# Kernel optimization log

Hardware: AMD Instinct MI355X
Metric: run time of the kernel (lower is better)

## Reference

```python
import jax, jax.numpy as jnp
import numpy as np
from jax import lax

K_DIM, E_DIM, H_DIM, BETA = 256, 64, 256, 0.25
DN = ('NCHW', 'OIHW', 'NCHW')


def conv(x, w, b=None, stride=1, pad=0):
    y = lax.conv_general_dilated(x, w, (stride, stride), [(pad, pad), (pad, pad)], dimension_numbers=DN)
    if b is not None:
        y = y + b[None, :, None, None]
    return y


def deconv(x, w, b):
    # torch ConvTranspose2d(k=4, stride=2, pad=1): weight [in, out, kH, kW]
    rhs = jnp.flip(w, (2, 3)).swapaxes(0, 1)  # -> [out, in, kH, kW]
    y = lax.conv_general_dilated(x, rhs, (1, 1), [(2, 2), (2, 2)], lhs_dilation=(2, 2), dimension_numbers=DN)
    return y + b[None, :, None, None]


def res_block(x, w3, w1):
    out = jax.nn.relu(x)
    out = conv(out, w3, stride=1, pad=1)
    out = jax.nn.relu(out)
    out = conv(out, w1, stride=1, pad=0)
    return out + x


def vq_embed(z, codebook):
    # z: [B, C, Hs, Ws]; faithful to original: flatten to (-1, e_dim) even though C != e_dim
    zp = jnp.transpose(z, (0, 2, 3, 1))  # [B,Hs,Ws,C]
    zf = zp.reshape(-1, E_DIM)  # [N, e_dim]
    # ||z||^2 + ||e||^2 - 2 z e^T
    dist = (jnp.sum(zf * zf, axis=1, keepdims=True)
            + jnp.sum(codebook * codebook, axis=1)
            - 2.0 * zf @ codebook.T)  # [N, K]
    idx = jnp.argmin(dist, axis=1)  # [N]
    vq = jnp.take(codebook, idx, axis=0).reshape(zp.shape)  # gather == one-hot matmul
    loss = (jnp.mean((lax.stop_gradient(vq) - zp) ** 2)
            + BETA * jnp.mean((vq - lax.stop_gradient(zp)) ** 2))
    vq_st = zp + lax.stop_gradient(vq - zp)  # straight-through
    return loss, jnp.transpose(vq_st, (0, 3, 1, 2))


def setup_inputs() -> dict:
    key = jax.random.key(0)
    ks = jax.random.split(key, 20)
    f32 = jnp.float32
    s = 0.05
    inp = {
        'x': jax.random.normal(ks[0], (32, 3, 128, 128), f32),
        'enc_w1': jax.random.normal(ks[1], (H_DIM, 3, 4, 4), f32) * s,
        'enc_b1': jnp.zeros((H_DIM,), f32),
        'enc_w2': jax.random.normal(ks[2], (H_DIM, H_DIM, 4, 4), f32) * s,
        'enc_b2': jnp.zeros((H_DIM,), f32),
        'er1_w3': jax.random.normal(ks[3], (H_DIM, H_DIM, 3, 3), f32) * s,
        'er1_w1': jax.random.normal(ks[4], (H_DIM, H_DIM, 1, 1), f32) * s,
        'er2_w3': jax.random.normal(ks[5], (H_DIM, H_DIM, 3, 3), f32) * s,
        'er2_w1': jax.random.normal(ks[6], (H_DIM, H_DIM, 1, 1), f32) * s,
        'codebook': jax.random.uniform(ks[7], (K_DIM, E_DIM), f32, -1.0 / K_DIM, 1.0 / K_DIM),
        'dr1_w3': jax.random.normal(ks[8], (H_DIM, H_DIM, 3, 3), f32) * s,
        'dr1_w1': jax.random.normal(ks[9], (H_DIM, H_DIM, 1, 1), f32) * s,
        'dr2_w3': jax.random.normal(ks[10], (H_DIM, H_DIM, 3, 3), f32) * s,
        'dr2_w1': jax.random.normal(ks[11], (H_DIM, H_DIM, 1, 1), f32) * s,
        'dt1_w': jax.random.normal(ks[12], (H_DIM, H_DIM, 4, 4), f32) * s,  # [in,out,k,k]
        'dt1_b': jnp.zeros((H_DIM,), f32),
        'dt2_w': jax.random.normal(ks[13], (H_DIM, 3, 4, 4), f32) * s,
        'dt2_b': jnp.zeros((3,), f32),
    }
    return inp


def reference(x, enc_w1, enc_b1, enc_w2, enc_b2, er1_w3, er1_w1, er2_w3, er2_w1,
              codebook, dr1_w3, dr1_w1, dr2_w3, dr2_w1, dt1_w, dt1_b, dt2_w, dt2_b):
    # encoder
    z = conv(x, enc_w1, enc_b1, stride=2, pad=1)
    z = conv(z, enc_w2, enc_b2, stride=2, pad=1)
    z = res_block(z, er1_w3, er1_w1)
    z = res_block(z, er2_w3, er2_w1)
    # VQ
    emb_loss, vq_z = vq_embed(z, codebook)
    # decoder
    d = res_block(vq_z, dr1_w3, dr1_w1)
    d = res_block(d, dr2_w3, dr2_w1)
    d = deconv(d, dt1_w, dt1_b)
    d = deconv(d, dt2_w, dt2_b)
    recon = jnp.tanh(d)
    return recon, emb_loss
```

## Files before the change

### kernel.cpp

```cpp
#include <hip/hip_runtime.h>
#include <math.h>


typedef unsigned short ushort;
typedef short bf16x8 __attribute__((ext_vector_type(8)));
typedef float f32x4 __attribute__((ext_vector_type(4)));

__device__ __forceinline__ ushort f2bf(float f) {
    unsigned u = __builtin_bit_cast(unsigned, f);
    unsigned r = (u + 0x7fffu + ((u >> 16) & 1u)) >> 16;
    return (ushort)r;
}
__device__ __forceinline__ float bfl(unsigned u) { return __builtin_bit_cast(float, u << 16); }
__device__ __forceinline__ float bfh(unsigned u) { return __builtin_bit_cast(float, u & 0xffff0000u); }

__device__ __forceinline__ unsigned relu_u(unsigned u) {
    unsigned m = (u >> 15) & 0x00010001u;
    return u & ~((m << 16) - m);
}
__device__ __forceinline__ uint4 relu4(uint4 v) {
    v.x = relu_u(v.x); v.y = relu_u(v.y); v.z = relu_u(v.z); v.w = relu_u(v.w);
    return v;
}

__global__ void k_pack_c3x4(const float* __restrict__ w0, const float* __restrict__ w1,
                            const float* __restrict__ w2, const float* __restrict__ w3,
                            ushort* __restrict__ o0, ushort* __restrict__ o1,
                            ushort* __restrict__ o2, ushort* __restrict__ o3) {
    int layer = blockIdx.x / 2304;
    int i = (blockIdx.x - layer * 2304) * 256 + threadIdx.x;
    const float* w = layer == 0 ? w0 : layer == 1 ? w1 : layer == 2 ? w2 : w3;
    ushort* o = layer == 0 ? o0 : layer == 1 ? o1 : layer == 2 ? o2 : o3;
    int kk = i & 31, co = (i >> 5) & 255, cb = (i >> 13) & 7, t = i >> 16;
    int ci = cb * 32 + kk, kh = t / 3, kw = t % 3;
    o[i] = f2bf(w[((co * 256 + ci) * 3 + kh) * 3 + kw]);
}

__global__ void k_pack_c1x1x4(const float* __restrict__ w0, const float* __restrict__ w1,
                              const float* __restrict__ w2, const float* __restrict__ w3,
                              ushort* __restrict__ o0, ushort* __restrict__ o1,
                              ushort* __restrict__ o2, ushort* __restrict__ o3) {
    int layer = blockIdx.x >> 8;
    int i = (blockIdx.x & 255) * 256 + threadIdx.x;
    const float* w = layer == 0 ? w0 : layer == 1 ? w1 : layer == 2 ? w2 : w3;
    ushort* o = layer == 0 ? o0 : layer == 1 ? o1 : layer == 2 ? o2 : o3;
    int kk = i & 31, co = (i >> 5) & 255, cb = (i >> 13) & 7;
    o[i] = f2bf(w[co * 256 + cb * 32 + kk]);
}

__global__ void k_pack_vq(const float* __restrict__ cb, ushort* __restrict__ apk,
                          float* __restrict__ en) {
    if (blockIdx.x < 64) {
        int i = blockIdx.x * 256 + threadIdx.x;
        int j = i & 7, lane = (i >> 3) & 63, s = (i >> 9) & 1, t = i >> 10;
        int code = t * 16 + (lane & 15);
        int dim = s * 32 + (lane >> 4) * 8 + j;
        apk[i] = f2bf(cb[code * 64 + dim]);
    } else {
        int code = threadIdx.x;
        float s = 0.f;
        for (int d = 0; d < 64; ++d) { float v = cb[code * 64 + d]; s += v * v; }
        en[code] = s;
    }
}

__global__ __launch_bounds__(256) void k_wcomp_enc(const float* __restrict__ w1,
                                                   const float* __restrict__ b1f,
                                                   const float* __restrict__ w2,
                                                   const float* __restrict__ b2f,
                                                   ushort* __restrict__ wenc,
                                                   float* __restrict__ benc,
                                                   float* __restrict__ wct,
                                                   float* __restrict__ wcb,
                                                   float* __restrict__ wcl,
                                                   float* __restrict__ wcr,
                                                   float* __restrict__ wcc) {
    __shared__ float sw1[12288];
    __shared__ float sw2[4096];
    __shared__ float part[2400];
    int co = blockIdx.x, tid = threadIdx.x;
    for (int i = tid; i < 12288; i += 256) sw1[i] = w1[i];
    for (int i = tid; i < 4096; i += 256) sw2[i] = w2[co * 4096 + i];
    __syncthreads();

    {
        float s = 0.f;
#pragma unroll
        for (int t = 0; t < 16; ++t) s += sw2[tid * 16 + t];
        float pb = b1f[tid] * s;
#pragma unroll
        for (int m = 1; m < 64; m <<= 1) pb += __shfl_xor(pb, m);
        if ((tid & 63) == 0) part[tid >> 6] = pb;
    }
    __syncthreads();
    if (tid == 0) benc[co] = b2f[co] + part[0] + part[1] + part[2] + part[3];

    if (tid < 240) {
        int y = tid / 24, rem = tid % 24, ci = rem / 8, ms = rem % 8;
        int na = 0, aa[2], h1[2];
#pragma unroll
        for (int a = 0; a < 4; ++a) {
            int k1 = y - 2 * a;
            if ((unsigned)k1 < 4u) { aa[na] = a; h1[na] = k1; ++na; }
        }
        float acc10[10];
#pragma unroll
        for (int xx = 0; xx < 10; ++xx) acc10[xx] = 0.f;
        for (int m = ms * 32; m < ms * 32 + 32; ++m) {
            for (int pa = 0; pa < na; ++pa) {
                float4 a2 = *(const float4*)&sw2[m * 16 + aa[pa] * 4];
                float4 a1 = *(const float4*)&sw1[m * 48 + ci * 16 + h1[pa] * 4];
                acc10[0] += a2.x * a1.x; acc10[1] += a2.x * a1.y; acc10[2] += a2.x * a1.z; acc10[3] += a2.x * a1.w;
                acc10[2] += a2.y * a1.x; acc10[3] += a2.y * a1.y; acc10[4] += a2.y * a1.z; acc10[5] += a2.y * a1.w;
                acc10[4] += a2.z * a1.x; acc10[5] += a2.z * a1.y; acc10[6] += a2.z * a1.z; acc10[7] += a2.z * a1.w;
                acc10[6] += a2.w * a1.x; acc10[7] += a2.w * a1.y; acc10[8] += a2.w * a1.z; acc10[9] += a2.w * a1.w;
            }
        }
#pragma unroll
        for (int xx = 0; xx < 10; ++xx) part[tid * 10 + xx] = acc10[xx];
    }
    __syncthreads();
    for (int w = tid; w < 320; w += 256) {
        if (w < 300) {
            int y = w / 30, r = w % 30, ci = r / 10, xx = r % 10;
            float s = 0.f;
#pragma unroll
            for (int ms = 0; ms < 8; ++ms) s += part[((y * 24 + ci * 8) + ms) * 10 + xx];
            wenc[(y * 256 + co) * 32 + xx * 3 + ci] = f2bf(s);
        } else {
            int j = w - 300;
            int y = j >> 1;
            wenc[(y * 256 + co) * 32 + 30 + (j & 1)] = 0;
        }
    }

    if (tid < 30 || (tid >= 32 && tid < 62)) {
        bool top = tid < 30;
        int t = top ? tid : tid - 32;
        int xx = t / 3, ci = t % 3;
        int k2hf = top ? 0 : 3, k1hf = top ? 3 : 0;
        float s = 0.f;
        for (int m = 0; m < 256; ++m)
            for (int k2w = 0; k2w < 4; ++k2w) {
                int k1w = xx - 2 * k2w;
                if ((unsigned)k1w < 4u)
                    s += sw2[m * 16 + k2hf * 4 + k2w] * sw1[m * 48 + ci * 16 + k1hf * 4 + k1w];
            }
        (top ? wct : wcb)[t * 256 + co] = s;
    } else if ((tid >= 64 && tid < 94) || (tid >= 96 && tid < 126)) {
        bool left = tid < 94;
        int t = left ? tid - 64 : tid - 96;
        int y = t / 3, ci = t % 3;
        int k2wf = left ? 0 : 3, k1wf = left ? 3 : 0;
        float s = 0.f;
        for (int m = 0; m < 256; ++m)
            for (int k2h = 0; k2h < 4; ++k2h) {
                int k1h = y - 2 * k2h;
                if ((unsigned)k1h < 4u)
                    s += sw2[m * 16 + k2h * 4 + k2wf] * sw1[m * 48 + ci * 16 + k1h * 4 + k1wf];
            }
        (left ? wcl : wcr)[t * 256 + co] = s;
    } else if (tid >= 128 && tid < 140) {
        int c = (tid - 128) / 3, ci = (tid - 128) % 3;
        int k2h = (c >> 1) ? 3 : 0, k2w = (c & 1) ? 3 : 0;
        int k1h = 3 - k2h, k1w = 3 - k2w;
        float s = 0.f;
        for (int m = 0; m < 256; ++m)
            s += sw2[m * 16 + k2h * 4 + k2w] * sw1[m * 48 + ci * 16 + k1h * 4 + k1w];
        wcc[(c * 3 + ci) * 256 + co] = s;
    }
}

__global__ __launch_bounds__(256) void k_wcomp_dec(const float* __restrict__ dt1,
                                                   const float* __restrict__ dt1b,
                                                   const float* __restrict__ dt2,
                                                   const float* __restrict__ dt2b,
                                                   ushort* __restrict__ wdec,
                                                   float* __restrict__ bdec) {
    __shared__ float s1[4096];
    __shared__ float s2[12288];
    __shared__ float part[2400];
    int ci = blockIdx.x, tid = threadIdx.x;
    for (int i = tid; i < 4096; i += 256) s1[i] = dt1[ci * 4096 + i];
    for (int i = tid; i < 12288; i += 256) s2[i] = dt2[i];
    __syncthreads();

    if (ci == 0 && tid < 48) {
        int o = tid >> 4, p = tid & 15, py = p >> 2, px = p & 3;
        int c0 = (py + 1) & 1, d0 = (px + 1) & 1;
        float s = dt2b[o];
        for (int m = 0; m < 256; ++m) {
            float t2 = s2[m * 48 + o * 16 + c0 * 4 + d0] + s2[m * 48 + o * 16 + c0 * 4 + d0 + 2]
                     + s2[m * 48 + o * 16 + (c0 + 2) * 4 + d0] + s2[m * 48 + o * 16 + (c0 + 2) * 4 + d0 + 2];
            s += dt1b[m] * t2;
        }
        bdec[tid] = s;
    }

    if (tid < 240) {
        int y = tid / 24, rem = tid % 24, o = rem / 8, ms = rem % 8;
        int na = 0, aa[2], cc[2];
#pragma unroll
        for (int a = 0; a < 4; ++a) {
            int c = y - 2 * a;
            if ((unsigned)c < 4u) { aa[na] = a; cc[na] = c; ++na; }
        }
        float acc10[10];
#pragma unroll
        for (int xx = 0; xx < 10; ++xx) acc10[xx] = 0.f;
        for (int m = ms * 32; m < ms * 32 + 32; ++m) {
            for (int pa = 0; pa < na; ++pa) {
                float4 d1 = *(const float4*)&s1[m * 16 + aa[pa] * 4];
                float4 d2 = *(const float4*)&s2[m * 48 + o * 16 + cc[pa] * 4];
                acc10[0] += d1.x * d2.x; acc10[1] += d1.x * d2.y; acc10[2] += d1.x * d2.z; acc10[3] += d1.x * d2.w;
                acc10[2] += d1.y * d2.x; acc10[3] += d1.y * d2.y; acc10[4] += d1.y * d2.z; acc10[5] += d1.y * d2.w;
                acc10[4] += d1.z * d2.x; acc10[5] += d1.z * d2.y; acc10[6] += d1.z * d2.z; acc10[7] += d1.z * d2.w;
                acc10[6] += d1.w * d2.x; acc10[7] += d1.w * d2.y; acc10[8] += d1.w * d2.z; acc10[9] += d1.w * d2.w;
            }
        }
#pragma unroll
        for (int xx = 0; xx < 10; ++xx) part[tid * 10 + xx] = acc10[xx];
    }
    __syncthreads();
    for (int w = tid; w < 300; w += 256) {
        int y = w / 30, r = w % 30, o = r / 10, xx = r % 10;
        float s = 0.f;
#pragma unroll
        for (int ms = 0; ms < 8; ++ms) s += part[((y * 24 + o * 8) + ms) * 10 + xx];
        int du = (y < 3) ? 1 : (y < 7) ? 0 : -1;
        int py = y - 3 + 4 * du;
        int dv = (xx < 3) ? 1 : (xx < 7) ? 0 : -1;
        int px = xx - 3 + 4 * dv;
        int t = (du + 1) * 3 + (dv + 1);
        int cb2 = ci >> 5, kk = ci & 31;
        wdec[((((t * 3 + o) * 8 + cb2) * 16 + py * 4 + px) * 32) + kk] = f2bf(s);
    }
}

__global__ void k_xpack(const float* __restrict__ x, ushort* __restrict__ xpk) {
    int i = blockIdx.x * 256 + threadIdx.x;
    int k = i & 31, ow = (i >> 5) & 31, r = (i >> 10) & 127, n = i >> 17;
    float v = 0.f;
    if (k < 30) {
        int ci = k % 3, kw = k / 3;
        int col = 4 * ow - 3 + kw;
        if ((unsigned)col < 128u) v = x[((n * 3 + ci) * 128 + r) * 128 + col];
    }
    xpk[i] = f2bf(v);
}

__global__ __launch_bounds__(128) void k_enc_comp(const ushort* __restrict__ xpk,
                                                  const ushort* __restrict__ wenc,
                                                  const float* __restrict__ benc,
                                                  ushort* __restrict__ obf) {
    int tid = threadIdx.x, lane = tid & 63, wv = tid >> 6;
    int q = lane >> 4, l15 = lane & 15;
    int b = blockIdx.x;
    int mblk = b & 7, coslab = (b >> 3) & 3, n = b >> 5;
    int R0 = mblk * 4 + wv * 2;
    int aoff = (coslab * 64 + l15) * 32 + q * 8;

    f32x4 acc[4][4];
#pragma unroll
    for (int at = 0; at < 4; ++at)
#pragma unroll
        for (int bt = 0; bt < 4; ++bt) acc[at][bt] = 0.f;

    for (int t = 0; t < 10; ++t) {
        bf16x8 af[4];
#pragma unroll
        for (int at = 0; at < 4; ++at)
            af[at] = *(const bf16x8*)(wenc + t * 8192 + aoff + at * 512);
#pragma unroll
        for (int bt2 = 0; bt2 < 2; ++bt2) {
            int irow = 4 * (R0 + bt2) + t - 3;
            if ((unsigned)irow >= 128u) continue;
            bf16x8 bf[2];
#pragma unroll
            for (int hb = 0; hb < 2; ++hb) {
                int ow = hb * 16 + l15;
                bf[hb] = *(const bf16x8*)(xpk + (((long)n * 128 + irow) * 32 + ow) * 32 + q * 8);
            }
#pragma unroll
            for (int at = 0; at < 4; ++at)
#pragma unroll
                for (int hb = 0; hb < 2; ++hb)
                    acc[at][bt2 * 2 + hb] = __builtin_amdgcn_mfma_f32_16x16x32_bf16(
                        af[at], bf[hb], acc[at][bt2 * 2 + hb], 0, 0, 0);
        }
    }

    int co_base = coslab * 64;
#pragma unroll
    for (int at = 0; at < 4; ++at) {
        int co_t = co_base + at * 16 + q * 4;
        float4 b4 = *(const float4*)(benc + co_t);
        float bv[4] = {b4.x, b4.y, b4.z, b4.w};
#pragma unroll
        for (int bt = 0; bt < 4; ++bt) {
            int m = R0 * 32 + bt * 16 + l15;
            long oaddr = ((long)n * 1024 + m) * 256 + co_t;
            float v[4];
#pragma unroll
            for (int r = 0; r < 4; ++r) v[r] = acc[at][bt][r] + bv[r];
            uint2 pk;
            pk.x = (unsigned)f2bf(v[0]) | ((unsigned)f2bf(v[1]) << 16);
            pk.y = (unsigned)f2bf(v[2]) | ((unsigned)f2bf(v[3]) << 16);
            *(uint2*)(obf + oaddr) = pk;
        }
    }
}

__global__ __launch_bounds__(256) void k_fix_border(const float* __restrict__ x,
                                                    const ushort* __restrict__ xpk,
                                                    const float* __restrict__ wct,
                                                    const float* __restrict__ wcb,
                                                    const float* __restrict__ wcl,
                                                    const float* __restrict__ wcr,
                                                    const float* __restrict__ wcc,
                                                    ushort* __restrict__ X0) {
    int b = blockIdx.x;
    int n = b >> 7, job = b & 127;
    if (job >= 124) return;
    int co = threadIdx.x;

    auto dot_tb = [&](const float* __restrict__ w, int row, int qq) -> float {
        const ushort* xr = xpk + (((long)n * 128 + row) * 32 + qq) * 32;
        float s = 0.f;
        for (int k = 0; k < 30; ++k) s += w[k * 256 + co] * bfl((unsigned)xr[k]);
        return s;
    };
    auto dot_lr = [&](const float* __restrict__ w, int p, int colofs) -> float {
        float s = 0.f;
        for (int y = 0; y < 10; ++y) {
            int row = 4 * p - 3 + y;
            if ((unsigned)row >= 128u) continue;
            for (int ci = 0; ci < 3; ++ci)
                s += w[(y * 3 + ci) * 256 + co] * x[((long)(n * 3 + ci) * 128 + row) * 128 + colofs];
        }
        return s;
    };
    auto corner = [&](int c, int row, int colofs) -> float {
        float s = 0.f;
        for (int ci = 0; ci < 3; ++ci)
            s += wcc[(c * 3 + ci) * 256 + co] * x[((long)(n * 3 + ci) * 128 + row) * 128 + colofs];
        return s;
    };

    int m;
    float corr;
    if (job < 32) {
        int qq = job;
        m = qq;
        corr = dot_tb(wct, 0, qq);
        if (qq == 0)  corr += dot_lr(wcl, 0, 0)   - corner(0, 0, 0);
        if (qq == 31) corr += dot_lr(wcr, 0, 127) - corner(1, 0, 127);
    } else if (job < 64) {
        int qq = job - 32;
        m = 992 + qq;
        corr = dot_tb(wcb, 127, qq);
        if (qq == 0)  corr += dot_lr(wcl, 31, 0)   - corner(2, 127, 0);
        if (qq == 31) corr += dot_lr(wcr, 31, 127) - corner(3, 127, 127);
    } else if (job < 94) {
        int p = job - 63;
        m = 32 * p;
        corr = dot_lr(wcl, p, 0);
    } else {
        int p = job - 93;
        m = 32 * p + 31;
        corr = dot_lr(wcr, p, 127);
    }

    ushort* ptr = X0 + ((long)n * 1024 + m) * 256 + co;
    float v = bfl((unsigned)(*ptr));
    *ptr = f2bf(v - corr);
}

__global__ __launch_bounds__(256, 2) void k_resblock(const ushort* __restrict__ xin,
                                                     const ushort* __restrict__ w3pk,
                                                     const ushort* __restrict__ w1pk,
                                                     ushort* __restrict__ obf) {
    constexpr int BUFU = 4 * 4 * 34 * 8;
    __shared__ __align__(16) ushort sX[2 * BUFU];
    __shared__ __align__(16) ushort sEx[64 * 256];

    int tid = threadIdx.x, lane = tid & 63, wv = tid >> 6;
    int q = lane >> 4, l15 = lane & 15;
    int b = blockIdx.x;
    int rp = b & 15, n = b >> 4;
    int R0 = rp * 2;

    if (tid < 64) {
        int bufi = tid >> 5, rq = (tid >> 1) & 15, cc = (tid & 1) ? 33 : 0;
        uint4 z; z.x = z.y = z.z = z.w = 0;
        *(uint4*)&sX[bufi * BUFU + (rq * 34 + cc) * 8] = z;
    }

    int brr[4], bcol[4];
#pragma unroll
    for (int bt = 0; bt < 4; ++bt) {
        int p = bt * 16 + l15;
        brr[bt] = p >> 5; bcol[bt] = (p & 31) + 1;
    }

    int scol = lane >> 1, j0 = (lane & 1) * 2;
    int aoff = (wv * 64 + l15) * 32 + q * 8;

    f32x4 acc[4][4];
#pragma unroll
    for (int at = 0; at < 4; ++at)
#pragma unroll
        for (int bt = 0; bt < 4; ++bt) acc[at][bt] = 0.f;

    int hh = R0 - 1 + wv;
    bool hvalid = (unsigned)hh < 32u;
    uint4 sreg[2];
    auto stage_load = [&](int cb2) {
        long off = (((long)n * 32 + hh) * 32 + scol) * 256 + cb2 * 32 + j0 * 8;
#pragma unroll
        for (int k = 0; k < 2; ++k) {
            uint4 v;
            if (hvalid) v = relu4(*(const uint4*)(xin + off + k * 8));
            else { v.x = 0; v.y = 0; v.z = 0; v.w = 0; }
            sreg[k] = v;
        }
    };
    auto write_stage = [&](int pbuf) {
        ushort* bufp = sX + pbuf * BUFU;
#pragma unroll
        for (int k = 0; k < 2; ++k)
            *(uint4*)&bufp[((wv * 4 + j0 + k) * 34 + scol + 1) * 8] = sreg[k];
    };

    stage_load(0);
    write_stage(0);
    __syncthreads();

    for (int cb = 0; cb < 8; ++cb) {
        ushort* bufp = sX + (cb & 1) * BUFU;
        if (cb + 1 < 8) stage_load(cb + 1);
        const ushort* wb = w3pk + (long)cb * 8192 + aoff;

        bf16x8 afc[4];
#pragma unroll
        for (int at = 0; at < 4; ++at) afc[at] = *(const bf16x8*)(wb + at * 512);
#pragma unroll
        for (int t = 0; t < 9; ++t) {
            bf16x8 afn[4];
            if (t < 8) {
#pragma unroll
                for (int at = 0; at < 4; ++at)
                    afn[at] = *(const bf16x8*)(wb + (long)(t + 1) * 65536 + at * 512);
            }
            int taprow = t / 3, dx = t % 3 - 1;
            bf16x8 bfr[4];
#pragma unroll
            for (int bt = 0; bt < 4; ++bt)
                bfr[bt] = *(const bf16x8*)&bufp[(((brr[bt] + taprow) * 4 + q) * 34 + bcol[bt] + dx) * 8];
#pragma unroll
            for (int at = 0; at < 4; ++at)
#pragma unroll
                for (int bt = 0; bt < 4; ++bt)
                    acc[at][bt] = __builtin_amdgcn_mfma_f32_16x16x32_bf16(afc[at], bfr[bt],
                                                                          acc[at][bt], 0, 0, 0);
            if (t < 8) {
#pragma unroll
                for (int at = 0; at < 4; ++at) afc[at] = afn[at];
            }
        }

        if (cb + 1 < 8) {
            write_stage((cb + 1) & 1);
            __syncthreads();
        }
    }

#pragma unroll
    for (int at = 0; at < 4; ++at) {
        int co_t = wv * 64 + at * 16 + q * 4;
#pragma unroll
        for (int bt = 0; bt < 4; ++bt) {
            int px = bt * 16 + l15;
            uint2 pk;
            pk.x = (unsigned)f2bf(fmaxf(acc[at][bt][0], 0.f))
                 | ((unsigned)f2bf(fmaxf(acc[at][bt][1], 0.f)) << 16);
            pk.y = (unsigned)f2bf(fmaxf(acc[at][bt][2], 0.f))
                 | ((unsigned)f2bf(fmaxf(acc[at][bt][3], 0.f)) << 16);
            *(uint2*)&sEx[px * 256 + (co_t ^ ((px & 7) << 3))] = pk;
        }
    }
    __syncthreads();

    f32x4 acc2[4][4];
#pragma unroll
    for (int at = 0; at < 4; ++at)
#pragma unroll
        for (int bt = 0; bt < 4; ++bt) acc2[at][bt] = 0.f;

    for (int cb = 0; cb < 8; ++cb) {
        const ushort* wb1 = w1pk + (long)cb * 8192 + aoff;
        bf16x8 af1[4];
#pragma unroll
        for (int at = 0; at < 4; ++at) af1[at] = *(const bf16x8*)(wb1 + at * 512);
        bf16x8 bf1[4];
#pragma unroll
        for (int bt = 0; bt < 4; ++bt) {
            int px = bt * 16 + l15;
            bf1[bt] = *(const bf16x8*)&sEx[px * 256 + ((cb * 32 + q * 8) ^ ((px & 7) << 3))];
        }
#pragma unroll
        for (int at = 0; at < 4; ++at)
#pragma unroll
            for (int bt = 0; bt < 4; ++bt)
                acc2[at][bt] = __builtin_amdgcn_mfma_f32_16x16x32_bf16(af1[at], bf1[bt],
                                                                      acc2[at][bt], 0, 0, 0);
    }

#pragma unroll
    for (int at = 0; at < 4; ++at) {
        int co_t = wv * 64 + at * 16 + q * 4;
#pragma unroll
        for (int bt = 0; bt < 4; ++bt) {
            int m = R0 * 32 + bt * 16 + l15;
            long oaddr = ((long)n * 1024 + m) * 256 + co_t;
            uint2 rr = *(const uint2*)(xin + oaddr);
            float v[4];
            v[0] = acc2[at][bt][0] + bfl(rr.x);
            v[1] = acc2[at][bt][1] + bfh(rr.x);
            v[2] = acc2[at][bt][2] + bfl(rr.y);
            v[3] = acc2[at][bt][3] + bfh(rr.y);
            uint2 pk;
            pk.x = (unsigned)f2bf(v[0]) | ((unsigned)f2bf(v[1]) << 16);
            pk.y = (unsigned)f2bf(v[2]) | ((unsigned)f2bf(v[3]) << 16);
            *(uint2*)(obf + oaddr) = pk;
        }
    }
}

__global__ __launch_bounds__(256) void k_vq2(const ushort* __restrict__ zb,
                                             const ushort* __restrict__ apk,
                                             const float* __restrict__ en,
                                             const float* __restrict__ cbf,
                                             ushort* __restrict__ vqb,
                                             float* __restrict__ loss) {
    __shared__ int sIdx[64];
    __shared__ float sLoss[64];
    int tid = threadIdx.x, lane = tid & 63, wv = tid >> 6;
    int q = lane >> 4, l15 = lane & 15;
    int r0 = blockIdx.x * 64;
    int R = r0 + wv * 16;

    const ushort* zp = zb + ((long)(R + l15)) * 64 + q * 8;
    bf16x8 b0 = *(const bf16x8*)zp;
    bf16x8 b1 = *(const bf16x8*)(zp + 32);

    float z2 = 0.f;
    {
        const unsigned* u0 = (const unsigned*)&b0;
        const unsigned* u1 = (const unsigned*)&b1;
#pragma unroll
        for (int i = 0; i < 4; ++i) {
            float a = bfl(u0[i]), bb = bfh(u0[i]);
            float c = bfl(u1[i]), d = bfh(u1[i]);
            z2 += a * a + bb * bb + c * c + d * d;
        }
    }

    float best = 3.4e38f;
    int bidx = 0;
#pragma unroll
    for (int t = 0; t < 16; ++t) {
        bf16x8 a0 = *(const bf16x8*)(apk + ((t * 2 + 0) * 64 + lane) * 8);
        bf16x8 a1 = *(const bf16x8*)(apk + ((t * 2 + 1) * 64 + lane) * 8);
        f32x4 acc = {0.f, 0.f, 0.f, 0.f};
        acc = __builtin_amdgcn_mfma_f32_16x16x32_bf16(a0, b0, acc, 0, 0, 0);
        acc = __builtin_amdgcn_mfma_f32_16x16x32_bf16(a1, b1, acc, 0, 0, 0);
        float4 e4 = *(const float4*)(en + t * 16 + q * 4);
        float sc[4] = {e4.x - 2.f * acc[0], e4.y - 2.f * acc[1],
                       e4.z - 2.f * acc[2], e4.w - 2.f * acc[3]};
#pragma unroll
        for (int r = 0; r < 4; ++r) {
            int code = t * 16 + q * 4 + r;
            if (sc[r] < best) { best = sc[r]; bidx = code; }
        }
    }
#pragma unroll
    for (int m = 16; m <= 32; m <<= 1) {
        float ob = __shfl_xor(best, m);
        int oi = __shfl_xor(bidx, m);
        if (ob < best || (ob == best && oi < bidx)) { best = ob; bidx = oi; }
        z2 += __shfl_xor(z2, m);
    }
    if (q == 0) {
        sIdx[wv * 16 + l15] = bidx;
        sLoss[wv * 16 + l15] = best + z2;
    }
    __syncthreads();

    if (wv == 0) {
        float l = sLoss[lane];
#pragma unroll
        for (int m = 1; m < 64; m <<= 1) l += __shfl_xor(l, m);
        if (lane == 0) atomicAdd(loss, l * (1.25f / 8388608.f));
    }

    unsigned* vb = (unsigned*)(vqb + (long)r0 * 64);
#pragma unroll
    for (int k = 0; k < 8; ++k) {
        int i = k * 256 + tid;
        int rl = i >> 5, jp = i & 31;
        int idx = sIdx[rl];
        float v0 = cbf[idx * 64 + 2 * jp];
        float v1 = cbf[idx * 64 + 2 * jp + 1];
        vb[i] = (unsigned)f2bf(v0) | ((unsigned)f2bf(v1) << 16);
    }
}

__global__ __launch_bounds__(128, 2) void k_dec_comp(const ushort* __restrict__ xin,
                                                     const ushort* __restrict__ wdec,
                                                     const float* __restrict__ bdec,
                                                     float* __restrict__ out) {
    constexpr int BUFU = 3 * 4 * 34 * 8;
    constexpr int WLDS = 2 * BUFU;
    __shared__ __align__(16) ushort sX[2 * WLDS];
    __shared__ __align__(16) float sOut[3072];

    int tid = threadIdx.x, lane = tid & 63, wv = tid >> 6;
    int q = lane >> 4, l15 = lane & 15;
    int b = blockIdx.x;
    int rp = b & 15, n = b >> 4;
    int U = rp * 2 + wv;
    ushort* sW = sX + wv * WLDS;

    if (lane < 48) {
        int cc = (lane & 1) ? 33 : 0;
        int sq = lane >> 1;
        uint4 z; z.x = z.y = z.z = z.w = 0;
        *(uint4*)&sW[(sq * 34 + cc) * 8] = z;
    }
    int scol = lane >> 1, j0 = (lane & 1) * 2;

    f32x4 acc[3][2];
#pragma unroll
    for (int o = 0; o < 3; ++o)
#pragma unroll
        for (int bt = 0; bt < 2; ++bt) acc[o][bt] = 0.f;

    uint4 sreg[3][2];
    auto stage_load = [&](int cb2) {
#pragma unroll
        for (int r = 0; r < 3; ++r) {
            int hh = U - 1 + r;
            bool valid = (unsigned)hh < 32u;
            long off = (((long)n * 32 + hh) * 32 + scol) * 256 + cb2 * 32 + j0 * 8;
#pragma unroll
            for (int k = 0; k < 2; ++k) {
                uint4 v;
                if (valid) v = *(const uint4*)(xin + off + k * 8);
                else { v.x = 0; v.y = 0; v.z = 0; v.w = 0; }
                sreg[r][k] = v;
            }
        }
    };
    auto write_stage = [&](int pbuf) {
        ushort* bufp = sW + pbuf * BUFU;
#pragma unroll
        for (int r = 0; r < 3; ++r)
#pragma unroll
            for (int k = 0; k < 2; ++k)
                *(uint4*)&bufp[((r * 4 + j0 + k) * 34 + scol + 1) * 8] = sreg[r][k];
    };

    stage_load(0);
    write_stage(0);

    for (int cb = 0; cb < 8; ++cb) {
        ushort* bufp = sW + (cb & 1) * BUFU;
        if (cb + 1 < 8) stage_load(cb + 1);
        const ushort* wb = wdec + (long)cb * 512 + l15 * 32 + q * 8;
#pragma unroll
        for (int t = 0; t < 9; ++t) {
            int du = t / 3 - 1, dv = t % 3 - 1;
            bf16x8 bfr[2];
#pragma unroll
            for (int bt = 0; bt < 2; ++bt)
                bfr[bt] = *(const bf16x8*)&bufp[(((du + 1) * 4 + q) * 34 + bt * 16 + l15 + 1 + dv) * 8];
#pragma unroll
            for (int o = 0; o < 3; ++o) {
                bf16x8 af = *(const bf16x8*)(wb + (long)(t * 3 + o) * 4096);
#pragma unroll
                for (int bt = 0; bt < 2; ++bt)
                    acc[o][bt] = __builtin_amdgcn_mfma_f32_16x16x32_bf16(af, bfr[bt], acc[o][bt], 0, 0, 0);
            }
        }
        if (cb + 1 < 8) write_stage((cb + 1) & 1);
    }

#pragma unroll
    for (int o = 0; o < 3; ++o) {
#pragma unroll
        for (int bt = 0; bt < 2; ++bt) {
            int V = bt * 16 + l15;
#pragma unroll
            for (int r = 0; r < 4; ++r) {
                int p = q * 4 + r, py = p >> 2, px = p & 3;
                sOut[((o * 2 + wv) * 4 + py) * 128 + 4 * V + px] =
                    tanhf(acc[o][bt][r] + bdec[o * 16 + p]);
            }
        }
    }
    __syncthreads();

#pragma unroll
    for (int i = 0; i < 6; ++i) {
        int idx = i * 128 + tid;
        int row = idx >> 5, colq = idx & 31;
        int o = row >> 3, rem = row & 7, wv2 = rem >> 2, py = rem & 3;
        long g = ((((long)n * 3 + o) * 128) + 4 * (rp * 2 + wv2) + py) * 128 + colq * 4;
        *(float4*)(out + g) = *(float4*)&sOut[row * 128 + colq * 4];
    }
}

extern "C" void kernel_launch(void* const* d_in, const int* in_sizes, int n_in,
                              void* d_out, int out_size, void* d_ws, size_t ws_size,
                              hipStream_t stream) {
    (void)in_sizes; (void)n_in; (void)out_size; (void)ws_size;
    const float* x        = (const float*)d_in[0];
    const float* enc_w1   = (const float*)d_in[1];
    const float* enc_b1   = (const float*)d_in[2];
    const float* enc_w2   = (const float*)d_in[3];
    const float* enc_b2   = (const float*)d_in[4];
    const float* er1_w3   = (const float*)d_in[5];
    const float* er1_w1   = (const float*)d_in[6];
    const float* er2_w3   = (const float*)d_in[7];
    const float* er2_w1   = (const float*)d_in[8];
    const float* codebook = (const float*)d_in[9];
    const float* dr1_w3   = (const float*)d_in[10];
    const float* dr1_w1   = (const float*)d_in[11];
    const float* dr2_w3   = (const float*)d_in[12];
    const float* dr2_w1   = (const float*)d_in[13];
    const float* dt1_w    = (const float*)d_in[14];
    const float* dt1_b    = (const float*)d_in[15];
    const float* dt2_w    = (const float*)d_in[16];
    const float* dt2_b    = (const float*)d_in[17];

    float* recon = (float*)d_out;
    float* loss  = recon + 1572864;

    char* ws = (char*)d_ws;
    size_t off = 0;
    auto alloc = [&](size_t bytes) { char* p = ws + off; off += (bytes + 255) & ~(size_t)255; return p; };
    ushort* X0   = (ushort*)alloc(16777216);
    ushort* X2   = (ushort*)alloc(16777216);
    ushort* X3   = (ushort*)alloc(16777216);
    ushort* X4   = (ushort*)alloc(16777216);
    ushort* xpk  = (ushort*)alloc(8388608);
    ushort* wpk_er13 = (ushort*)alloc(1179648);
    ushort* wpk_er23 = (ushort*)alloc(1179648);
    ushort* wpk_dr13 = (ushort*)alloc(1179648);
    ushort* wpk_dr23 = (ushort*)alloc(1179648);
    ushort* wpk_er11 = (ushort*)alloc(131072);
    ushort* wpk_er21 = (ushort*)alloc(131072);
    ushort* wpk_dr11 = (ushort*)alloc(131072);
    ushort* wpk_dr21 = (ushort*)alloc(131072);
    ushort* wenc     = (ushort*)alloc(163840);
    ushort* wdec     = (ushort*)alloc(221184);
    ushort* apk      = (ushort*)alloc(32768);
    float*  benc     = (float*)alloc(1024);
    float*  bdec     = (float*)alloc(192);
    float*  en       = (float*)alloc(1024);
    float*  wct      = (float*)alloc(32768);
    float*  wcb      = (float*)alloc(32768);
    float*  wcl      = (float*)alloc(32768);
    float*  wcr      = (float*)alloc(32768);
    float*  wcc      = (float*)alloc(12288);

    hipMemsetAsync(loss, 0, sizeof(float), stream);
    hipMemsetAsync(wdec, 0, 221184, stream);

    k_pack_c3x4<<<9216, 256, 0, stream>>>(er1_w3, er2_w3, dr1_w3, dr2_w3,
                                          wpk_er13, wpk_er23, wpk_dr13, wpk_dr23);
    k_pack_c1x1x4<<<1024, 256, 0, stream>>>(er1_w1, er2_w1, dr1_w1, dr2_w1,
                                            wpk_er11, wpk_er21, wpk_dr11, wpk_dr21);
    k_pack_vq<<<65, 256, 0, stream>>>(codebook, apk, en);
    k_wcomp_enc<<<256, 256, 0, stream>>>(enc_w1, enc_b1, enc_w2, enc_b2, wenc, benc,
                                         wct, wcb, wcl, wcr, wcc);
    k_wcomp_dec<<<256, 256, 0, stream>>>(dt1_w, dt1_b, dt2_w, dt2_b, wdec, bdec);
    k_xpack<<<16384, 256, 0, stream>>>(x, xpk);

    k_enc_comp<<<1024, 128, 0, stream>>>(xpk, wenc, benc, X0);
    k_fix_border<<<4096, 256, 0, stream>>>(x, xpk, wct, wcb, wcl, wcr, wcc, X0);
    k_resblock<<<512, 256, 0, stream>>>(X0, wpk_er13, wpk_er11, X2);
    k_resblock<<<512, 256, 0, stream>>>(X2, wpk_er23, wpk_er21, X3);
    k_vq2<<<2048, 256, 0, stream>>>(X3, apk, en, codebook, X4, loss);
    k_resblock<<<512, 256, 0, stream>>>(X4, wpk_dr13, wpk_dr11, X0);
    k_resblock<<<512, 256, 0, stream>>>(X0, wpk_dr23, wpk_dr21, X2);
    k_dec_comp<<<512, 128, 0, stream>>>(X2, wdec, bdec, recon);
}
```

Measured before the change: 546.4 us.

## Relayout packed input for coalesced loads and deepen weight prefetch in res-block MFMA loops

```diff
diff --git a/kernel.cpp b/kernel.cpp
--- a/kernel.cpp
+++ b/kernel.cpp
@@ -239,7 +239,8 @@
 
 __global__ void k_xpack(const float* __restrict__ x, ushort* __restrict__ xpk) {
     int i = blockIdx.x * 256 + threadIdx.x;
-    int k = i & 31, ow = (i >> 5) & 31, r = (i >> 10) & 127, n = i >> 17;
+    int j = i & 7, ow = (i >> 3) & 31, q = (i >> 8) & 3, r = (i >> 10) & 127, n = i >> 17;
+    int k = q * 8 + j;
     float v = 0.f;
     if (k < 30) {
         int ci = k % 3, kw = k / 3;
@@ -279,7 +280,7 @@
 #pragma unroll
             for (int hb = 0; hb < 2; ++hb) {
                 int ow = hb * 16 + l15;
-                bf[hb] = *(const bf16x8*)(xpk + (((long)n * 128 + irow) * 32 + ow) * 32 + q * 8);
+                bf[hb] = *(const bf16x8*)(xpk + ((((long)n * 128 + irow) * 4 + q) * 32 + ow) * 8);
             }
 #pragma unroll
             for (int at = 0; at < 4; ++at)
@@ -325,9 +326,10 @@
     int co = threadIdx.x;
 
     auto dot_tb = [&](const float* __restrict__ w, int row, int qq) -> float {
-        const ushort* xr = xpk + (((long)n * 128 + row) * 32 + qq) * 32;
+        const ushort* xr = xpk + ((long)n * 128 + row) * 1024;
         float s = 0.f;
-        for (int k = 0; k < 30; ++k) s += w[k * 256 + co] * bfl((unsigned)xr[k]);
+        for (int k = 0; k < 30; ++k)
+            s += w[k * 256 + co] * bfl((unsigned)xr[(k >> 3) * 256 + qq * 8 + (k & 7)]);
         return s;
     };
     auto dot_lr = [&](const float* __restrict__ w, int p, int colofs) -> float {
@@ -434,23 +436,33 @@
 
     stage_load(0);
     write_stage(0);
+
+    bf16x8 afA[3][4];
+    {
+        const ushort* wb0 = w3pk + aoff;
+#pragma unroll
+        for (int at = 0; at < 4; ++at) afA[0][at] = *(const bf16x8*)(wb0 + at * 512);
+#pragma unroll
+        for (int at = 0; at < 4; ++at) afA[1][at] = *(const bf16x8*)(wb0 + 65536 + at * 512);
+    }
     __syncthreads();
 
     for (int cb = 0; cb < 8; ++cb) {
         ushort* bufp = sX + (cb & 1) * BUFU;
         if (cb + 1 < 8) stage_load(cb + 1);
         const ushort* wb = w3pk + (long)cb * 8192 + aoff;
-
-        bf16x8 afc[4];
-#pragma unroll
-        for (int at = 0; at < 4; ++at) afc[at] = *(const bf16x8*)(wb + at * 512);
+        const ushort* wbn = w3pk + (long)(cb + 1) * 8192 + aoff;
+
 #pragma unroll
         for (int t = 0; t < 9; ++t) {
-            bf16x8 afn[4];
-            if (t < 8) {
+            if (t < 7) {
 #pragma unroll
                 for (int at = 0; at < 4; ++at)
-                    afn[at] = *(const bf16x8*)(wb + (long)(t + 1) * 65536 + at * 512);
+                    afA[(t + 2) % 3][at] = *(const bf16x8*)(wb + (long)(t + 2) * 65536 + at * 512);
+            } else if (cb < 7) {
+#pragma unroll
+                for (int at = 0; at < 4; ++at)
+                    afA[(t + 2) % 3][at] = *(const bf16x8*)(wbn + (long)(t - 7) * 65536 + at * 512);
             }
             int taprow = t / 3, dx = t % 3 - 1;
             bf16x8 bfr[4];
@@ -461,12 +473,8 @@
             for (int at = 0; at < 4; ++at)
 #pragma unroll
                 for (int bt = 0; bt < 4; ++bt)
-                    acc[at][bt] = __builtin_amdgcn_mfma_f32_16x16x32_bf16(afc[at], bfr[bt],
+                    acc[at][bt] = __builtin_amdgcn_mfma_f32_16x16x32_bf16(afA[t % 3][at], bfr[bt],
                                                                           acc[at][bt], 0, 0, 0);
-            if (t < 8) {
-#pragma unroll
-                for (int at = 0; at < 4; ++at) afc[at] = afn[at];
-            }
         }
 
         if (cb + 1 < 8) {
@@ -497,11 +505,16 @@
 #pragma unroll
         for (int bt = 0; bt < 4; ++bt) acc2[at][bt] = 0.f;
 
+    bf16x8 af1c[4], af1n[4];
+#pragma unroll
+    for (int at = 0; at < 4; ++at) af1c[at] = *(const bf16x8*)(w1pk + aoff + at * 512);
+
     for (int cb = 0; cb < 8; ++cb) {
-        const ushort* wb1 = w1pk + (long)cb * 8192 + aoff;
-        bf16x8 af1[4];
-#pragma unroll
-        for (int at = 0; at < 4; ++at) af1[at] = *(const bf16x8*)(wb1 + at * 512);
+        if (cb + 1 < 8) {
+            const ushort* wb1n = w1pk + (long)(cb + 1) * 8192 + aoff;
+#pragma unroll
+            for (int at = 0; at < 4; ++at) af1n[at] = *(const bf16x8*)(wb1n + at * 512);
+        }
         bf16x8 bf1[4];
 #pragma unroll
         for (int bt = 0; bt < 4; ++bt) {
@@ -512,8 +525,12 @@
         for (int at = 0; at < 4; ++at)
 #pragma unroll
             for (int bt = 0; bt < 4; ++bt)
-                acc2[at][bt] = __builtin_amdgcn_mfma_f32_16x16x32_bf16(af1[at], bf1[bt],
+                acc2[at][bt] = __builtin_amdgcn_mfma_f32_16x16x32_bf16(af1c[at], bf1[bt],
                                                                       acc2[at][bt], 0, 0, 0);
+        if (cb + 1 < 8) {
+#pragma unroll
+            for (int at = 0; at < 4; ++at) af1c[at] = af1n[at];
+        }
     }
 
 #pragma unroll
```

Result: faster. 534.1 us (-2.3%).
